# Performance work log

Measured on AMD Instinct MI355X. Metric: run time of the kernel, lower is better.

Reference implementation:

```python
import jax, jax.numpy as jnp
import numpy as np

B, S, D, H, SE, DE, DFF = 4, 1024, 1024, 16, 77, 768, 4096


def _ln(x, g, b, eps=1e-5):
    mu = jnp.mean(x, axis=-1, keepdims=True)
    var = jnp.mean((x - mu) ** 2, axis=-1, keepdims=True)
    return (x - mu) * jax.lax.rsqrt(var + eps) * g + b


def _split_heads(x, heads):
    b, s, d = x.shape
    return x.reshape(b, s, heads, d // heads).transpose(0, 2, 1, 3)  # b h s hd


def _attn(q, k, v, heads):
    # memory_efficient_attention equivalent: softmax(q k^T * scale) v, per head
    q, k, v = _split_heads(q, heads), _split_heads(k, heads), _split_heads(v, heads)
    scale = q.shape[-1] ** -0.5
    scores = jnp.einsum('bhqd,bhkd->bhqk', q, k) * scale
    probs = jax.nn.softmax(scores, axis=-1)
    o = jnp.einsum('bhqk,bhkd->bhqd', probs, v)
    b, h, s, hd = o.shape
    return o.transpose(0, 2, 1, 3).reshape(b, s, h * hd)


def _geglu_ff(x, w1, b1, w2, b2):
    proj = x @ w1 + b1
    a, gate = jnp.split(proj, 2, axis=-1)
    return (a * jax.nn.gelu(gate)) @ w2 + b2


def _forward(h1, h2, enc, wq, wk, wv, wqc, wo, bo, ln1g, ln1b, ln2g, ln2b,
             w2q, w2k, w2v, w2o, b2o, wff1, bff1, wff2, bff2):
    # norm1
    n1 = _ln(h1, ln1g[0], ln1b[0])
    n2 = _ln(h2, ln1g[1], ln1b[1])
    # dual-stream uni-direction attention (self + cross with swapped K/V)
    q1, k1, v1, q1c = n1 @ wq[0], n1 @ wk[0], n1 @ wv[0], n1 @ wqc[0]
    q2, k2, v2, q2c = n2 @ wq[1], n2 @ wk[1], n2 @ wv[1], n2 @ wqc[1]
    a1 = _attn(q1, k1, v1, H) + _attn(q1c, k2, v2, H)
    a2 = _attn(q2, k2, v2, H) + _attn(q2c, k1, v1, H)
    a1 = a1 @ wo[0] + bo[0]
    a2 = a2 @ wo[1] + bo[1]
    h1 = h1 + a1
    h2 = h2 + a2
    # cross attention to encoder states (attn2)
    n1 = _ln(h1, ln2g[0], ln2b[0])
    n2 = _ln(h2, ln2g[1], ln2b[1])
    c1 = _attn(n1 @ w2q[0], enc @ w2k[0], enc @ w2v[0], H) @ w2o[0] + b2o[0]
    c2 = _attn(n2 @ w2q[1], enc @ w2k[1], enc @ w2v[1], H) @ w2o[1] + b2o[1]
    h1 = h1 + c1
    h2 = h2 + c2
    # feed-forward (GEGLU), applied to norm2 output exactly as in source
    h1 = h1 + _geglu_ff(n1, wff1[0], bff1[0], wff2[0], bff2[0])
    h2 = h2 + _geglu_ff(n2, wff1[1], bff1[1], wff2[1], bff2[1])
    return (h1, h2)


def setup_inputs() -> dict:
    key = jax.random.key(0)
    ks = jax.random.split(key, 16)
    f = lambda k, shp: jax.random.normal(k, shp, jnp.float32) * 0.02
    return {
        'h1': jax.random.normal(ks[0], (B, S, D), jnp.float32),
        'h2': jax.random.normal(ks[1], (B, S, D), jnp.float32),
        'enc': jax.random.normal(ks[2], (B, SE, DE), jnp.float32),
        'wq': f(ks[3], (2, D, D)), 'wk': f(ks[4], (2, D, D)),
        'wv': f(ks[5], (2, D, D)), 'wqc': f(ks[6], (2, D, D)),
        'wo': f(ks[7], (2, D, D)), 'bo': jnp.zeros((2, D), jnp.float32),
        'ln1g': jnp.ones((2, D), jnp.float32), 'ln1b': jnp.zeros((2, D), jnp.float32),
        'ln2g': jnp.ones((2, D), jnp.float32), 'ln2b': jnp.zeros((2, D), jnp.float32),
        'w2q': f(ks[8], (2, D, D)), 'w2k': f(ks[9], (2, DE, D)),
        'w2v': f(ks[10], (2, DE, D)), 'w2o': f(ks[11], (2, D, D)),
        'b2o': jnp.zeros((2, D), jnp.float32),
        'wff1': f(ks[12], (2, D, 2 * DFF)), 'bff1': jnp.zeros((2, 2 * DFF), jnp.float32),
        'wff2': f(ks[13], (2, DFF, D)), 'bff2': jnp.zeros((2, D), jnp.float32),
    }


def reference(h1, h2, enc, wq, wk, wv, wqc, wo, bo, ln1g, ln1b, ln2g, ln2b,
              w2q, w2k, w2v, w2o, b2o, wff1, bff1, wff2, bff2):
    return _forward(h1, h2, enc, wq, wk, wv, wqc, wo, bo, ln1g, ln1b, ln2g, ln2b,
                    w2q, w2k, w2v, w2o, b2o, wff1, bff1, wff2, bff2)
```

## Files before the change

### kernel.cpp

```cpp
#include <hip/hip_runtime.h>

typedef unsigned short u16;
typedef short v8s __attribute__((ext_vector_type(8)));
typedef float v4f __attribute__((ext_vector_type(4)));

__device__ __forceinline__ float bf2f(u16 u) {
  union { unsigned u; float f; } c; c.u = ((unsigned)u) << 16; return c.f;
}
__device__ __forceinline__ u16 f2bf(float x) {
  union { float f; unsigned u; } c; c.f = x;
  unsigned r = c.u + 0x7fffu + ((c.u >> 16) & 1u);
  return (u16)(r >> 16);
}
__device__ __forceinline__ v4f vzero() { v4f z; z[0]=0.f; z[1]=0.f; z[2]=0.f; z[3]=0.f; return z; }
__device__ __forceinline__ v4f mfma16(v8s a, v8s b, v4f c) {
  return __builtin_amdgcn_mfma_f32_16x16x32_bf16(a, b, c, 0, 0, 0);
}
__device__ __forceinline__ void async_lds16(const void* g, void* l) {
  __builtin_amdgcn_global_load_lds((__attribute__((address_space(1))) void*)g,
                                   (__attribute__((address_space(3))) void*)l, 16, 0, 0);
}
__device__ __forceinline__ unsigned cvtpk(float lo, float hi) {
  unsigned r;
  asm("v_cvt_pk_bf16_f32 %0, %1, %2" : "=v"(r) : "v"(lo), "v"(hi));
  return r;
}
__device__ __forceinline__ float gelu_f(float x) {
  return 0.5f * x * (1.f + tanhf(0.7978845608028654f * (x + 0.044715f * x * x * x)));
}

__global__ void detect_k(const unsigned* __restrict__ p, unsigned* __restrict__ flag) {
  if (threadIdx.x == 0) {
    flag[0] = (p[0] == 0x3F803F80u) ? 1u : 0u;
    flag[1] = 0u;
  }
}

__global__ __launch_bounds__(256) void cvt_k(const unsigned* __restrict__ flag,
    const void* __restrict__ src, u16* __restrict__ dst, int n) {
  int i = (blockIdx.x * 256 + threadIdx.x) * 8;
  if (i >= n) return;
  if (*flag) {
    *(uint4*)(dst + i) = *(const uint4*)((const u16*)src + i);
  } else {
    const float* s = (const float*)src + i;
    #pragma unroll
    for (int j = 0; j < 8; ++j) dst[i + j] = f2bf(s[j]);
  }
}

__global__ __launch_bounds__(256) void tr_k(const unsigned* __restrict__ flag,
    const void* __restrict__ in, u16* __restrict__ out, int R, int C, long outZS) {
  __shared__ u16 tile[32][33];
  size_t zin = (size_t)blockIdx.z * R * C;
  size_t zout = (size_t)blockIdx.z * outZS;
  int c0 = blockIdx.x * 32, r0 = blockIdx.y * 32;
  int tx = threadIdx.x & 31, ty = threadIdx.x >> 5;
  unsigned isbf = *flag;
  const u16* inb = (const u16*)in + zin;
  const float* inf = (const float*)in + zin;
  #pragma unroll
  for (int i = ty; i < 32; i += 8) {
    size_t idx = (size_t)(r0 + i) * C + c0 + tx;
    tile[i][tx] = isbf ? inb[idx] : f2bf(inf[idx]);
  }
  __syncthreads();
  out += zout;
  #pragma unroll
  for (int i = ty; i < 32; i += 8) out[(size_t)(c0 + i) * R + r0 + tx] = tile[tx][i];
}

__global__ __launch_bounds__(256) void vtr_k(const u16* __restrict__ in, u16* __restrict__ out) {
  __shared__ u16 tile[32][33];
  int z = blockIdx.z >> 2, b = blockIdx.z & 3;
  const u16* ip = in + (size_t)z * 16777216 + (size_t)b * 4194304 + 2048;
  u16* op = out + (size_t)z * 4194304 + (size_t)b * 1048576;
  int k0 = blockIdx.x * 32, d0 = blockIdx.y * 32;
  int tx = threadIdx.x & 31, ty = threadIdx.x >> 5;
  #pragma unroll
  for (int i = ty; i < 32; i += 8)
    tile[i][tx] = ip[(size_t)(k0 + i) * 4096 + d0 + tx];
  __syncthreads();
  int sl = (((tx >> 3) & 1) << 4) | (((tx >> 2) & 1) << 3) | (((tx >> 4) & 1) << 2) | (tx & 3);
  #pragma unroll
  for (int i = ty; i < 32; i += 8)
    op[(size_t)(d0 + i) * 1024 + k0 + sl] = tile[tx][i];
}

__global__ __launch_bounds__(256) void ln_k(const unsigned* __restrict__ flag,
    const void* __restrict__ src0, const void* __restrict__ src1,
    const u16* __restrict__ gw, const u16* __restrict__ bw, u16* __restrict__ out) {
  int z = blockIdx.y;
  const void* src = z ? src1 : src0;
  out += (size_t)z * 4194304; gw += z * 1024; bw += z * 1024;
  int row = blockIdx.x, t = threadIdx.x;
  unsigned isbf = *flag;
  float4 v;
  if (isbf) {
    uint2 d = ((const uint2*)((const u16*)src + (size_t)row * 1024))[t];
    v.x = bf2f((u16)(d.x & 0xffffu)); v.y = bf2f((u16)(d.x >> 16));
    v.z = bf2f((u16)(d.y & 0xffffu)); v.w = bf2f((u16)(d.y >> 16));
  } else {
    v = ((const float4*)((const float*)src + (size_t)row * 1024))[t];
  }
  float s = v.x + v.y + v.z + v.w;
  float s2 = v.x * v.x + v.y * v.y + v.z * v.z + v.w * v.w;
  #pragma unroll
  for (int o = 32; o; o >>= 1) { s += __shfl_down(s, o); s2 += __shfl_down(s2, o); }
  __shared__ float red[8];
  int w = t >> 6;
  if ((t & 63) == 0) { red[w] = s; red[4 + w] = s2; }
  __syncthreads();
  if (t == 0) {
    red[0] = red[0] + red[1] + red[2] + red[3];
    red[4] = red[4] + red[5] + red[6] + red[7];
  }
  __syncthreads();
  float mu = red[0] * (1.f / 1024.f);
  float var = red[4] * (1.f / 1024.f) - mu * mu;
  float rstd = rsqrtf(var + 1e-5f);
  int c = t * 4;
  float xs[4] = { v.x, v.y, v.z, v.w };
  #pragma unroll
  for (int j = 0; j < 4; ++j) {
    float g = bf2f(gw[c + j]), bb = bf2f(bw[c + j]);
    out[(size_t)row * 1024 + c + j] = f2bf((xs[j] - mu) * rstd * g + bb);
  }
}

template<int EPI>
__global__ __launch_bounds__(256, 2) void gemm_bt(
    const u16* __restrict__ A, const u16* __restrict__ Bt,
    int M, int N, int K, int lda, int ldb, int ldc,
    const u16* __restrict__ bias, const u16* aux,
    float* __restrict__ resF, void* __restrict__ outB,
    long zsA, long zsB, long zsC, int zsBias,
    const void* rin0, const void* rin1,
    const unsigned* __restrict__ flagp)
{
  int z = blockIdx.z;
  A += (size_t)z * zsA;
  Bt += (size_t)z * zsB;
  size_t zc = (size_t)z * zsC;
  unsigned isbf = 0;
  if (EPI == 4 || EPI == 5) isbf = *flagp;
  const void* rin = (EPI == 5) ? (z ? rin1 : rin0) : nullptr;
  __shared__ alignas(16) u16 As[128 * 64];
  __shared__ alignas(16) u16 Bs[128 * 64];
  int tid = threadIdx.x;
  int lane = tid & 63, wave = tid >> 6;
  int l15 = lane & 15, l4 = lane >> 4;
  int wm = wave & 1, wn = wave >> 1;
  int lin = blockIdx.x + blockIdx.y * gridDim.x;
  int nxy = gridDim.x * gridDim.y;
  int sw = (lin & 7) * (nxy >> 3) + (lin >> 3);
  int bx = sw % gridDim.x, by = sw / gridDim.x;
  int m0 = bx * 128, n0 = by * 128;
  v4f acc[4][4];
  #pragma unroll
  for (int i = 0; i < 4; ++i)
    #pragma unroll
    for (int j = 0; j < 4; ++j) acc[i][j] = vzero();

  for (int k0 = 0; k0 < K; k0 += 64) {
    #pragma unroll
    for (int it = 0; it < 4; ++it) {
      int sidx = it * 256 + tid;
      int r = sidx >> 3, cs = (sidx & 7) * 8;
      int ra = m0 + r; if (ra > M - 1) ra = M - 1;
      async_lds16(A + (size_t)ra * lda + k0 + cs, As + (size_t)(it * 256 + wave * 64) * 8);
      async_lds16(Bt + (size_t)(n0 + r) * ldb + k0 + cs, Bs + (size_t)(it * 256 + wave * 64) * 8);
    }
    __syncthreads();
    #pragma unroll
    for (int ks = 0; ks < 2; ++ks) {
      v8s af[4], bfr[4];
      #pragma unroll
      for (int i = 0; i < 4; ++i) {
        af[i]  = *(const v8s*)(As + (wm * 64 + i * 16 + l15) * 64 + ks * 32 + l4 * 8);
        bfr[i] = *(const v8s*)(Bs + (wn * 64 + i * 16 + l15) * 64 + ks * 32 + l4 * 8);
      }
      #pragma unroll
      for (int i = 0; i < 4; ++i)
        #pragma unroll
        for (int j = 0; j < 4; ++j)
          acc[i][j] = mfma16(af[i], bfr[j], acc[i][j]);
    }
    __syncthreads();
  }
  #pragma unroll
  for (int mt = 0; mt < 4; ++mt) {
    #pragma unroll
    for (int r = 0; r < 4; ++r) {
      int gr = m0 + wm * 64 + mt * 16 + l4 * 4 + r;
      if (gr >= M) continue;
      size_t ri = (size_t)gr * ldc;
      size_t ro = zc + ri;
      #pragma unroll
      for (int nt = 0; nt < 4; ++nt) {
        int gc = n0 + wn * 64 + nt * 16 + l15;
        float v = acc[mt][nt][r];
        if (bias) v += bf2f(bias[(size_t)z * zsBias + gc]);
        if (EPI == 0) ((u16*)outB)[ro + gc] = f2bf(v);
        else if (EPI == 1) ((u16*)outB)[ro + gc] = f2bf(gelu_f(v));
        else if (EPI == 2) ((u16*)outB)[ro + gc] = f2bf(v * bf2f(aux[ro + gc]));
        else if (EPI == 3) resF[ro + gc] += v;
        else if (EPI == 5) {
          float h = isbf ? bf2f(((const u16*)rin)[ri + gc]) : ((const float*)rin)[ri + gc];
          resF[ro + gc] = h + v;
        } else {
          float o = resF[ro + gc] + v;
          if (isbf) ((u16*)outB)[ro + gc] = f2bf(o);
          else ((float*)outB)[ro + gc] = o;
        }
      }
    }
  }
}

template<int EPI>
__global__ __launch_bounds__(512, 2) void gemm256(
    const u16* __restrict__ A, const u16* __restrict__ Bt,
    int M, int N, int K, int lda, int ldb, int ldc,
    const u16* __restrict__ bias, const u16* aux, void* __restrict__ outB,
    long zsA, long zsB, long zsC, int zsBias)
{
  __shared__ alignas(16) u16 As[4][8192];
  __shared__ alignas(16) u16 Bs[4][8192];
  int z = blockIdx.z;
  A += (size_t)z * zsA;
  Bt += (size_t)z * zsB;
  size_t zc = (size_t)z * zsC;
  int tid = threadIdx.x, lane = tid & 63, wave = tid >> 6;
  int l15 = lane & 15, l4 = lane >> 4;
  int wm = wave >> 2, wn = wave & 3;
  int lin = blockIdx.x + blockIdx.y * gridDim.x;
  int nxy = gridDim.x * gridDim.y;
  int sw = (lin & 7) * (nxy >> 3) + (lin >> 3);
  int bx = sw % gridDim.x, by = sw / gridDim.x;
  int m0 = bx * 256, n0 = by * 256;
  int sa = l4 ^ ((l15 >> 1) & 3);
  int nG = K >> 5;

  v4f acc[8][4];
  #pragma unroll
  for (int i = 0; i < 8; ++i)
    #pragma unroll
    for (int j = 0; j < 4; ++j) acc[i][j] = vzero();

  auto stage = [&](int g) {
    int sl = g & 3;
    #pragma unroll
    for (int l = 0; l < 2; ++l) {
      int sidx = l * 512 + tid;
      int r = sidx >> 2, c = sidx & 3;
      int cs = (c ^ ((sidx >> 3) & 3)) * 8;
      async_lds16(A + (size_t)(m0 + r) * lda + g * 32 + cs,
                  As[sl] + (size_t)(l * 512 + wave * 64) * 8);
      async_lds16(Bt + (size_t)(n0 + r) * ldb + g * 32 + cs,
                  Bs[sl] + (size_t)(l * 512 + wave * 64) * 8);
    }
  };
  auto gate = [&](int cnt) {
    if (cnt >= 2)      asm volatile("s_waitcnt vmcnt(8)" ::: "memory");
    else if (cnt == 1) asm volatile("s_waitcnt vmcnt(4)" ::: "memory");
    else               asm volatile("s_waitcnt vmcnt(0)" ::: "memory");
    __builtin_amdgcn_sched_barrier(0);
  };
  v8s FA[8], FB[8], Bf[4];
  auto dsA = [&](v8s* F, int u) {
    const u16* a = As[u & 3];
    #pragma unroll
    for (int i = 0; i < 8; ++i)
      F[i] = *(const v8s*)(a + ((wm * 128 + i * 16 + l15) * 4 + sa) * 8);
  };
  auto dsB = [&](int u) {
    const u16* bp = Bs[u & 3];
    #pragma unroll
    for (int j = 0; j < 4; ++j)
      Bf[j] = *(const v8s*)(bp + ((wn * 64 + j * 16 + l15) * 4 + sa) * 8);
  };
  auto lgk = [&](bool more) {
    if (more) asm volatile("s_waitcnt lgkmcnt(8)" ::: "memory");
    else      asm volatile("s_waitcnt lgkmcnt(0)" ::: "memory");
    __builtin_amdgcn_sched_barrier(0);
  };
  auto mfma_blk = [&](v8s* F) {
    __builtin_amdgcn_s_setprio(1);
    #pragma unroll
    for (int i = 0; i < 8; ++i)
      #pragma unroll
      for (int j = 0; j < 4; ++j) acc[i][j] = mfma16(F[i], Bf[j], acc[i][j]);
    __builtin_amdgcn_s_setprio(0);
  };

  stage(0);
  if (1 < nG) stage(1);
  if (2 < nG) stage(2);
  gate((1 < nG) + (2 < nG));
  __builtin_amdgcn_s_barrier();
  dsA(FA, 0);

  for (int u = 0; u < nG; u += 2) {
    if (u + 3 < nG) stage(u + 3);
    gate((u + 2 < nG) + (u + 3 < nG));
    __builtin_amdgcn_s_barrier();
    dsB(u);
    if (u + 1 < nG) dsA(FB, u + 1);
    lgk(u + 1 < nG);
    mfma_blk(FA);
    __builtin_amdgcn_s_barrier();
    if (u + 1 < nG) {
      if (u + 4 < nG) stage(u + 4);
      gate((u + 3 < nG) + (u + 4 < nG));
      __builtin_amdgcn_s_barrier();
      dsB(u + 1);
      if (u + 2 < nG) dsA(FA, u + 2);
      lgk(u + 2 < nG);
      mfma_blk(FB);
      __builtin_amdgcn_s_barrier();
    }
  }

  #pragma unroll
  for (int mi = 0; mi < 8; ++mi) {
    #pragma unroll
    for (int rr = 0; rr < 4; ++rr) {
      int gr = m0 + wm * 128 + mi * 16 + l4 * 4 + rr;
      size_t ro = zc + (size_t)gr * ldc;
      #pragma unroll
      for (int ni = 0; ni < 4; ++ni) {
        int gc = n0 + wn * 64 + ni * 16 + l15;
        float v = acc[mi][ni][rr];
        if (bias) v += bf2f(bias[(size_t)z * zsBias + gc]);
        if (EPI == 0) ((u16*)outB)[ro + gc] = f2bf(v);
        else if (EPI == 1) ((u16*)outB)[ro + gc] = f2bf(gelu_f(v));
        else ((u16*)outB)[ro + gc] = f2bf(v * bf2f(aux[ro + gc]));
      }
    }
  }
}

__global__ __launch_bounds__(256, 4) void flash_self_k(
    const u16* __restrict__ qkv, const u16* __restrict__ Vt, u16* __restrict__ O)
{
  __shared__ alignas(16) u16 Ksh[128 * 64];
  __shared__ alignas(16) u16 Vsh[64 * 128];
  int tid = threadIdx.x, lane = tid & 63, wave = tid >> 6;
  int l15 = lane & 15, l4 = (lane >> 4) & 3;
  int lin = blockIdx.x + (blockIdx.y << 4) + (blockIdx.z << 8);
  int sw = (lin & 7) * 256 + (lin >> 3);
  int qblk = sw & 15, h = (sw >> 4) & 15, zb = sw >> 8;
  int strm = zb >> 2, b = zb & 3;
  const size_t ZS = 16777216;
  const size_t BS = 4194304;
  int q0 = qblk * 64 + wave * 16;
  int swz = l15 & 7;
  v4f res[4];
  #pragma unroll
  for (int i = 0; i < 4; ++i) res[i] = vzero();

  for (int sg = 0; sg < 2; ++sg) {
    int qcol = sg ? 3072 : 0;
    int ksrc = sg ? (strm ^ 1) : strm;
    const u16* Qb = qkv + (size_t)strm * ZS + (size_t)b * BS + qcol + h * 64;
    const u16* Kb = qkv + (size_t)ksrc * ZS + (size_t)b * BS + 1024 + h * 64;
    const u16* Vb = Vt + (size_t)ksrc * BS + (size_t)b * 1048576 + h * 65536;
    v8s qf0 = *(const v8s*)(Qb + (size_t)(q0 + l15) * 4096 + l4 * 8);
    v8s qf1 = *(const v8s*)(Qb + (size_t)(q0 + l15) * 4096 + l4 * 8 + 32);
    v4f oacc[4];
    #pragma unroll
    for (int i = 0; i < 4; ++i) oacc[i] = vzero();
    float mrun = -1e30f, lrun = 0.f;

    for (int c0 = 0; c0 < 1024; c0 += 128) {
      #pragma unroll
      for (int it = 0; it < 4; ++it) {
        int sidx = it * 256 + tid;
        int r = sidx >> 3, c = sidx & 7;
        async_lds16(Kb + (size_t)(c0 + r) * 4096 + ((c ^ (r & 7)) * 8),
                    Ksh + (size_t)(it * 256 + wave * 64) * 8);
      }
      #pragma unroll
      for (int it = 0; it < 4; ++it) {
        int sidx = it * 256 + tid;
        int d = sidx >> 4, c = sidx & 15;
        async_lds16(Vb + (size_t)d * 1024 + c0 + ((c ^ (d & 15)) * 8),
                    Vsh + (size_t)(it * 256 + wave * 64) * 8);
      }
      __syncthreads();
      v4f s[4][2];
      #pragma unroll
      for (int g = 0; g < 4; ++g) { s[g][0] = vzero(); s[g][1] = vzero(); }
      __builtin_amdgcn_s_setprio(1);
      #pragma unroll
      for (int g = 0; g < 4; ++g) {
        int rb0 = (g * 32 + l15) * 64, rb1 = rb0 + 16 * 64;
        v8s k00 = *(const v8s*)(Ksh + rb0 + ((l4 ^ swz) * 8));
        v8s k10 = *(const v8s*)(Ksh + rb1 + ((l4 ^ swz) * 8));
        v8s k01 = *(const v8s*)(Ksh + rb0 + (((4 + l4) ^ swz) * 8));
        v8s k11 = *(const v8s*)(Ksh + rb1 + (((4 + l4) ^ swz) * 8));
        s[g][0] = mfma16(k00, qf0, s[g][0]);
        s[g][1] = mfma16(k10, qf0, s[g][1]);
        s[g][0] = mfma16(k01, qf1, s[g][0]);
        s[g][1] = mfma16(k11, qf1, s[g][1]);
      }
      __builtin_amdgcn_s_setprio(0);
      float tm = -1e30f;
      #pragma unroll
      for (int g = 0; g < 4; ++g)
        #pragma unroll
        for (int hh = 0; hh < 2; ++hh)
          #pragma unroll
          for (int r = 0; r < 4; ++r) {
            s[g][hh][r] *= 0.125f;
            tm = fmaxf(tm, s[g][hh][r]);
          }
      tm = fmaxf(tm, __shfl_xor(tm, 16));
      tm = fmaxf(tm, __shfl_xor(tm, 32));
      float alpha = 1.f;
      if (!__all(tm <= mrun + 8.f)) {
        float mn = fmaxf(mrun, tm);
        alpha = __expf(mrun - mn);
        mrun = mn;
        #pragma unroll
        for (int r = 0; r < 4; ++r) {
          float ar = __shfl(alpha, l4 * 4 + r);
          #pragma unroll
          for (int nt = 0; nt < 4; ++nt) oacc[nt][r] *= ar;
        }
      }
      float rs = 0.f;
      unsigned pk[4][4];
      #pragma unroll
      for (int g = 0; g < 4; ++g)
        #pragma unroll
        for (int hh = 0; hh < 2; ++hh) {
          float p0 = __expf(s[g][hh][0] - mrun);
          float p1 = __expf(s[g][hh][1] - mrun);
          float p2 = __expf(s[g][hh][2] - mrun);
          float p3 = __expf(s[g][hh][3] - mrun);
          rs += (p0 + p1) + (p2 + p3);
          pk[g][hh * 2]     = cvtpk(p0, p1);
          pk[g][hh * 2 + 1] = cvtpk(p2, p3);
        }
      rs += __shfl_xor(rs, 16);
      rs += __shfl_xor(rs, 32);
      lrun = lrun * alpha + rs;
      __builtin_amdgcn_s_setprio(1);
      #pragma unroll
      for (int g = 0; g < 4; ++g) {
        union { unsigned u[4]; v8s v; } pa;
        pa.u[0] = pk[g][0]; pa.u[1] = pk[g][1]; pa.u[2] = pk[g][2]; pa.u[3] = pk[g][3];
        #pragma unroll
        for (int nt = 0; nt < 4; ++nt) {
          int vr = nt * 16 + l15;
          v8s vb = *(const v8s*)(Vsh + vr * 128 + (((g * 4 + l4) ^ (vr & 15)) * 8));
          oacc[nt] = mfma16(pa.v, vb, oacc[nt]);
        }
      }
      __builtin_amdgcn_s_setprio(0);
      __syncthreads();
    }
    #pragma unroll
    for (int r = 0; r < 4; ++r) {
      float lr = __shfl(lrun, l4 * 4 + r);
      float inv = 1.f / lr;
      #pragma unroll
      for (int nt = 0; nt < 4; ++nt) res[nt][r] += oacc[nt][r] * inv;
    }
  }
  #pragma unroll
  for (int nt = 0; nt < 4; ++nt) {
    #pragma unroll
    for (int r = 0; r < 4; ++r) {
      int gq = q0 + l4 * 4 + r;
      size_t oi = (size_t)strm * BS + ((size_t)b * 1024 + gq) * 1024 + h * 64 + nt * 16 + l15;
      O[oi] = f2bf(res[nt][r]);
    }
  }
}

__global__ __launch_bounds__(256, 2) void flash_cross_k(
    const u16* __restrict__ Q, const u16* __restrict__ KV, u16* __restrict__ O)
{
  __shared__ alignas(16) u16 Ksh[128 * 64];
  __shared__ alignas(16) unsigned VshT[64 * 68];
  __shared__ alignas(16) u16 Psh[4][16 * 128];
  int tid = threadIdx.x, lane = tid & 63, wave = tid >> 6;
  int l15 = lane & 15, l4 = lane >> 4;
  int h = blockIdx.y;
  int strm = blockIdx.z >> 2, b = blockIdx.z & 3;
  const u16* Qb = Q + (size_t)strm * 4194304 + (size_t)b * 1048576 + h * 64;
  const u16* Kb = KV + (size_t)strm * 630784 + (size_t)b * 157696 + h * 64;
  const u16* Vb = Kb + 1024;
  int q0 = blockIdx.x * 64 + wave * 16;
  u16* pw = Psh[wave];
  int swz = l15 & 7;
  v8s qf0 = *(const v8s*)(Qb + (size_t)(q0 + l15) * 1024 + l4 * 8);
  v8s qf1 = *(const v8s*)(Qb + (size_t)(q0 + l15) * 1024 + l4 * 8 + 32);

  #pragma unroll
  for (int it = 0; it < 4; ++it) {
    int sidx = it * 256 + tid;
    int r = sidx >> 3, c = sidx & 7;
    int gk = r > 76 ? 76 : r;
    async_lds16(Kb + (size_t)gk * 2048 + ((c ^ (r & 7)) * 8),
                Ksh + (size_t)(it * 256 + wave * 64) * 8);
  }
  #pragma unroll
  for (int it = 0; it < 2; ++it) {
    int tt = it * 256 + tid;
    int kp = tt & 63, dsg = tt >> 6;
    int gk0 = kp * 2, gk1 = kp * 2 + 1;
    if (gk0 > 76) gk0 = 76;
    if (gk1 > 76) gk1 = 76;
    v8s v0 = *(const v8s*)(Vb + (size_t)gk0 * 2048 + dsg * 8);
    v8s v1 = *(const v8s*)(Vb + (size_t)gk1 * 2048 + dsg * 8);
    #pragma unroll
    for (int j = 0; j < 8; ++j) {
      unsigned pk = (unsigned)(u16)v0[j] | ((unsigned)(u16)v1[j] << 16);
      VshT[(dsg * 8 + j) * 68 + kp] = pk;
    }
  }
  __syncthreads();
  v4f s[4][2];
  #pragma unroll
  for (int g = 0; g < 4; ++g) { s[g][0] = vzero(); s[g][1] = vzero(); }
  __builtin_amdgcn_s_setprio(1);
  #pragma unroll
  for (int g = 0; g < 4; ++g) {
    int rb0 = (g * 32 + l15) * 64, rb1 = rb0 + 16 * 64;
    v8s k00 = *(const v8s*)(Ksh + rb0 + ((l4 ^ swz) * 8));
    v8s k10 = *(const v8s*)(Ksh + rb1 + ((l4 ^ swz) * 8));
    v8s k01 = *(const v8s*)(Ksh + rb0 + (((4 + l4) ^ swz) * 8));
    v8s k11 = *(const v8s*)(Ksh + rb1 + (((4 + l4) ^ swz) * 8));
    s[g][0] = mfma16(qf0, k00, s[g][0]);
    s[g][1] = mfma16(qf0, k10, s[g][1]);
    s[g][0] = mfma16(qf1, k01, s[g][0]);
    s[g][1] = mfma16(qf1, k11, s[g][1]);
  }
  __builtin_amdgcn_s_setprio(0);
  float lsum[4];
  #pragma unroll
  for (int r = 0; r < 4; ++r) {
    int row = l4 * 4 + r;
    float x[8];
    #pragma unroll
    for (int g = 0; g < 4; ++g) {
      bool ok0 = (g * 32 + l15) < 77, ok1 = (g * 32 + 16 + l15) < 77;
      x[2 * g]     = ok0 ? s[g][0][r] * 0.125f : -1e30f;
      x[2 * g + 1] = ok1 ? s[g][1][r] * 0.125f : -1e30f;
    }
    float tm = fmaxf(fmaxf(fmaxf(x[0], x[1]), fmaxf(x[2], x[3])),
                     fmaxf(fmaxf(x[4], x[5]), fmaxf(x[6], x[7])));
    #pragma unroll
    for (int o = 8; o; o >>= 1) tm = fmaxf(tm, __shfl_xor(tm, o));
    float rs = 0.f;
    #pragma unroll
    for (int j = 0; j < 8; ++j) {
      float p = __expf(x[j] - tm);
      rs += p;
      int col = (j >> 1) * 32 + (j & 1) * 16 + l15;
      pw[row * 128 + (((col >> 3) ^ row) * 8) + (col & 7)] = f2bf(p);
    }
    #pragma unroll
    for (int o = 8; o; o >>= 1) rs += __shfl_xor(rs, o);
    lsum[r] = rs;
  }
  v4f oacc[4];
  #pragma unroll
  for (int i = 0; i < 4; ++i) oacc[i] = vzero();
  __builtin_amdgcn_s_setprio(1);
  #pragma unroll
  for (int g = 0; g < 4; ++g) {
    v8s pa = *(const v8s*)(pw + l15 * 128 + (((g * 4 + l4) ^ l15) * 8));
    #pragma unroll
    for (int nt = 0; nt < 4; ++nt) {
      v8s vb = *(const v8s*)((const u16*)VshT + (nt * 16 + l15) * 136 + g * 32 + l4 * 8);
      oacc[nt] = mfma16(pa, vb, oacc[nt]);
    }
  }
  __builtin_amdgcn_s_setprio(0);
  #pragma unroll
  for (int nt = 0; nt < 4; ++nt) {
    #pragma unroll
    for (int r = 0; r < 4; ++r) {
      int gq = q0 + l4 * 4 + r;
      size_t oi = (size_t)strm * 4194304 + ((size_t)b * 1024 + gq) * 1024 + h * 64 + nt * 16 + l15;
      O[oi] = f2bf(oacc[nt][r] / lsum[r]);
    }
  }
}

extern "C" void kernel_launch(void* const* d_in, const int* in_sizes, int n_in,
                              void* d_out, int out_size, void* d_ws, size_t ws_size,
                              hipStream_t stream)
{
  (void)in_sizes; (void)n_in; (void)out_size;
  const void* h1   = d_in[0];
  const void* h2   = d_in[1];
  const void* enc  = d_in[2];
  const void* wq   = d_in[3];
  const void* wk   = d_in[4];
  const void* wv   = d_in[5];
  const void* wqc  = d_in[6];
  const void* wo   = d_in[7];
  const void* bo   = d_in[8];
  const void* ln1g = d_in[9];
  const void* ln1b = d_in[10];
  const void* ln2g = d_in[11];
  const void* ln2b = d_in[12];
  const void* w2q  = d_in[13];
  const void* w2k  = d_in[14];
  const void* w2v  = d_in[15];
  const void* w2o  = d_in[16];
  const void* b2o  = d_in[17];
  const void* wff1 = d_in[18];
  const void* bff1 = d_in[19];
  const void* wff2 = d_in[20];
  const void* bff2 = d_in[21];

  const size_t S1 = 4194304;
  const size_t W1 = 1048576;
  const size_t QS = 16777216;
  const size_t NE = 236544;

  char* base = (char*)d_ws;
  size_t off = 0;
  auto AL = [&](size_t n) { size_t r = off; off += (n + 255) & ~(size_t)255; return r; };
  size_t o_flag   = AL(256);
  size_t o_pb     = AL(30720 * 2);
  size_t o_encB   = AL(NE * 2);
  size_t o_wqkvT  = AL(2 * 4 * W1 * 2);
  size_t o_woT    = AL(2 * W1 * 2);
  size_t o_w2qT   = AL(2 * W1 * 2);
  size_t o_w2oT   = AL(2 * W1 * 2);
  size_t o_w2kvT  = AL(2 * 2048 * 768 * 2);
  size_t o_wff1T  = AL(2 * 8192 * 1024 * 2);
  size_t o_wff2T  = AL(2 * 4096 * 1024 * 2);
  size_t o_hw     = AL(2 * S1 * 4);
  size_t o_n      = AL(2 * S1 * 2);
  size_t o_qkv    = AL(2 * QS * 2);
  size_t o_ab     = AL(2 * S1 * 2);
  if (ws_size < off) return;

  unsigned* flagp = (unsigned*)(base + o_flag);
  const unsigned* zerop = flagp + 1;
  u16* pb = (u16*)(base + o_pb);
  u16* boB   = pb + 0;
  u16* b2oB  = pb + 2048;
  u16* ln1gB = pb + 4096;
  u16* ln1bB = pb + 6144;
  u16* ln2gB = pb + 8192;
  u16* ln2bB = pb + 10240;
  u16* bff2B = pb + 12288;
  u16* bff1B = pb + 14336;
  u16* encB  = (u16*)(base + o_encB);
  u16* wqkvT = (u16*)(base + o_wqkvT);
  u16* woT   = (u16*)(base + o_woT);
  u16* w2qT  = (u16*)(base + o_w2qT);
  u16* w2oT  = (u16*)(base + o_w2oT);
  u16* w2kvT = (u16*)(base + o_w2kvT);
  u16* wff1T = (u16*)(base + o_wff1T);
  u16* wff2T = (u16*)(base + o_wff2T);
  float* hw  = (float*)(base + o_hw);
  u16* n1    = (u16*)(base + o_n);
  u16* qkv   = (u16*)(base + o_qkv);
  u16* a1b   = (u16*)(base + o_ab);
  u16* q1x   = qkv;
  u16* c1b   = qkv + 2 * S1;
  u16* kencv = qkv + 4 * S1;
  u16* gelu  = qkv;
  u16* vtb   = n1;

  auto tr = [&](const void* ip, u16* op, int R, int C, long outZS) {
    dim3 g(C / 32, R / 32, 2);
    tr_k<<<g, 256, 0, stream>>>(flagp, ip, op, R, C, outZS);
  };
  auto cvt = [&](const void* ip, u16* op, int n) {
    cvt_k<<<(n / 8 + 255) / 256, 256, 0, stream>>>(flagp, ip, op, n);
  };
  auto gemm = [&](int epi, const u16* Ap, const u16* Bp, int M, int N, int K,
                  int lda, int ldb, int ldc, const u16* bias, const u16* aux,
                  float* resF, void* oB, int nz, long zsA, long zsB, long zsC, int zsBias,
                  const void* rin0, const void* rin1) {
    dim3 g((M + 127) / 128, N / 128, nz);
    switch (epi) {
      case 0: gemm_bt<0><<<g, 256, 0, stream>>>(Ap, Bp, M, N, K, lda, ldb, ldc, bias, aux, resF, oB, zsA, zsB, zsC, zsBias, rin0, rin1, flagp); break;
      case 1: gemm_bt<1><<<g, 256, 0, stream>>>(Ap, Bp, M, N, K, lda, ldb, ldc, bias, aux, resF, oB, zsA, zsB, zsC, zsBias, rin0, rin1, flagp); break;
      case 2: gemm_bt<2><<<g, 256, 0, stream>>>(Ap, Bp, M, N, K, lda, ldb, ldc, bias, aux, resF, oB, zsA, zsB, zsC, zsBias, rin0, rin1, flagp); break;
      case 3: gemm_bt<3><<<g, 256, 0, stream>>>(Ap, Bp, M, N, K, lda, ldb, ldc, bias, aux, resF, oB, zsA, zsB, zsC, zsBias, rin0, rin1, flagp); break;
      case 4: gemm_bt<4><<<g, 256, 0, stream>>>(Ap, Bp, M, N, K, lda, ldb, ldc, bias, aux, resF, oB, zsA, zsB, zsC, zsBias, rin0, rin1, flagp); break;
      default: gemm_bt<5><<<g, 256, 0, stream>>>(Ap, Bp, M, N, K, lda, ldb, ldc, bias, aux, resF, oB, zsA, zsB, zsC, zsBias, rin0, rin1, flagp); break;
    }
  };

  detect_k<<<1, 64, 0, stream>>>((const unsigned*)ln1g, flagp);
  cvt(bo, boB, 2048);     cvt(b2o, b2oB, 2048);
  cvt(ln1g, ln1gB, 2048); cvt(ln1b, ln1bB, 2048);
  cvt(ln2g, ln2gB, 2048); cvt(ln2b, ln2bB, 2048);
  cvt(bff2, bff2B, 2048); cvt(bff1, bff1B, 16384);
  cvt(enc, encB, (int)NE);
  tr(wq,  wqkvT + 0 * W1, 1024, 1024, 4 * (long)W1);
  tr(wk,  wqkvT + 1 * W1, 1024, 1024, 4 * (long)W1);
  tr(wv,  wqkvT + 2 * W1, 1024, 1024, 4 * (long)W1);
  tr(wqc, wqkvT + 3 * W1, 1024, 1024, 4 * (long)W1);
  tr(wo,  woT,  1024, 1024, (long)W1);
  tr(w2q, w2qT, 1024, 1024, (long)W1);
  tr(w2o, w2oT, 1024, 1024, (long)W1);
  tr(w2k, w2kvT + 0,          768, 1024, 2048L * 768);
  tr(w2v, w2kvT + 1024 * 768, 768, 1024, 2048L * 768);
  tr(wff1, wff1T, 1024, 8192, 8192L * 1024);
  tr(wff2, wff2T, 4096, 1024, 4096L * 1024);
  ln_k<<<dim3(4096, 2), 256, 0, stream>>>(flagp, h1, h2, ln1gB, ln1bB, n1);
  gemm256<0><<<dim3(16, 16, 2), 512, 0, stream>>>(n1, wqkvT, 4096, 4096, 1024,
      1024, 1024, 4096, nullptr, nullptr, qkv, (long)S1, 4 * (long)W1, (long)QS, 0);
  vtr_k<<<dim3(32, 32, 8), 256, 0, stream>>>(qkv, vtb);
  flash_self_k<<<dim3(16, 16, 8), 256, 0, stream>>>(qkv, vtb, a1b);
  gemm(5, a1b, woT, 4096, 1024, 1024, 1024, 1024, 1024, boB, nullptr, hw, nullptr,
       2, (long)S1, (long)W1, (long)S1, 1024, h1, h2);
  ln_k<<<dim3(4096, 2), 256, 0, stream>>>(zerop, hw, hw + S1, ln2gB, ln2bB, n1);
  gemm(0, n1, w2qT, 4096, 1024, 1024, 1024, 1024, 1024, nullptr, nullptr, nullptr, q1x,
       2, (long)S1, (long)W1, (long)S1, 0, nullptr, nullptr);
  gemm(0, encB, w2kvT, 308, 2048, 768, 768, 768, 2048, nullptr, nullptr, nullptr, kencv,
       2, 0, 2048L * 768, 308L * 2048, 0, nullptr, nullptr);
  flash_cross_k<<<dim3(16, 16, 8), 256, 0, stream>>>(q1x, kencv, c1b);
  gemm(3, c1b, w2oT, 4096, 1024, 1024, 1024, 1024, 1024, b2oB, nullptr, hw, nullptr,
       2, (long)S1, (long)W1, (long)S1, 1024, nullptr, nullptr);
  gemm256<1><<<dim3(16, 16, 2), 512, 0, stream>>>(n1, wff1T + 4096 * 1024, 4096, 4096, 1024,
      1024, 1024, 4096, bff1B + 4096, nullptr, gelu, (long)S1, 8192L * 1024, (long)QS, 8192);
  gemm256<2><<<dim3(16, 16, 2), 512, 0, stream>>>(n1, wff1T, 4096, 4096, 1024,
      1024, 1024, 4096, bff1B, gelu, gelu, (long)S1, 8192L * 1024, (long)QS, 8192);
  gemm(4, gelu, wff2T, 4096, 1024, 4096, 4096, 4096, 1024,
       bff2B, nullptr, hw, d_out, 2, (long)QS, 4096L * 1024, (long)S1, 1024,
       nullptr, nullptr);
}
```

Measured before the change: 1.198 ms.

## Restructure gemm256 main loop into K-64 double-buffered eight-phase schedule

Replaces the four-slot K-32 ring buffer in the 256x256 GEMM with a double-buffered K-64 tile. Each tile is split into two K-32 halves, and each half into two M halves, giving four compute phases per tile. Global-to-LDS async loads for later tiles are interleaved between the phases, and each wave keeps only four A fragments live instead of two sets of eight, which lowers register pressure. The cost is more barriers and full lgkmcnt waits per tile. The loop also assumes K is a multiple of 64.

```diff
diff --git a/kernel.cpp b/kernel.cpp
--- a/kernel.cpp
+++ b/kernel.cpp
@@ -225,8 +225,8 @@
     const u16* __restrict__ bias, const u16* aux, void* __restrict__ outB,
     long zsA, long zsB, long zsC, int zsBias)
 {
-  __shared__ alignas(16) u16 As[4][8192];
-  __shared__ alignas(16) u16 Bs[4][8192];
+  __shared__ alignas(16) u16 Asl[2][2][256 * 32];
+  __shared__ alignas(16) u16 Bsl[2][2][256 * 32];
   int z = blockIdx.z;
   A += (size_t)z * zsA;
   Bt += (size_t)z * zsB;
@@ -240,7 +240,7 @@
   int bx = sw % gridDim.x, by = sw / gridDim.x;
   int m0 = bx * 256, n0 = by * 256;
   int sa = l4 ^ ((l15 >> 1) & 3);
-  int nG = K >> 5;
+  int Kt = K >> 6;
 
   v4f acc[8][4];
   #pragma unroll
@@ -248,78 +248,90 @@
     #pragma unroll
     for (int j = 0; j < 4; ++j) acc[i][j] = vzero();
 
-  auto stage = [&](int g) {
-    int sl = g & 3;
+  auto stA = [&](int g, int ks) {
+    u16* dst = Asl[g & 1][ks];
     #pragma unroll
     for (int l = 0; l < 2; ++l) {
       int sidx = l * 512 + tid;
       int r = sidx >> 2, c = sidx & 3;
-      int cs = (c ^ ((sidx >> 3) & 3)) * 8;
-      async_lds16(A + (size_t)(m0 + r) * lda + g * 32 + cs,
-                  As[sl] + (size_t)(l * 512 + wave * 64) * 8);
-      async_lds16(Bt + (size_t)(n0 + r) * ldb + g * 32 + cs,
-                  Bs[sl] + (size_t)(l * 512 + wave * 64) * 8);
-    }
-  };
-  auto gate = [&](int cnt) {
-    if (cnt >= 2)      asm volatile("s_waitcnt vmcnt(8)" ::: "memory");
-    else if (cnt == 1) asm volatile("s_waitcnt vmcnt(4)" ::: "memory");
-    else               asm volatile("s_waitcnt vmcnt(0)" ::: "memory");
+      async_lds16(A + (size_t)(m0 + r) * lda + g * 64 + ks * 32 + ((c ^ ((r >> 1) & 3)) * 8),
+                  dst + (size_t)(l * 512 + wave * 64) * 8);
+    }
+  };
+  auto stB = [&](int g, int ks) {
+    u16* dst = Bsl[g & 1][ks];
+    #pragma unroll
+    for (int l = 0; l < 2; ++l) {
+      int sidx = l * 512 + tid;
+      int r = sidx >> 2, c = sidx & 3;
+      async_lds16(Bt + (size_t)(n0 + r) * ldb + g * 64 + ks * 32 + ((c ^ ((r >> 1) & 3)) * 8),
+                  dst + (size_t)(l * 512 + wave * 64) * 8);
+    }
+  };
+  auto gate = [&](bool deep) {
+    if (deep) asm volatile("s_waitcnt vmcnt(6)" ::: "memory");
+    else      asm volatile("s_waitcnt vmcnt(0)" ::: "memory");
     __builtin_amdgcn_sched_barrier(0);
   };
-  v8s FA[8], FB[8], Bf[4];
-  auto dsA = [&](v8s* F, int u) {
-    const u16* a = As[u & 3];
-    #pragma unroll
-    for (int i = 0; i < 8; ++i)
-      F[i] = *(const v8s*)(a + ((wm * 128 + i * 16 + l15) * 4 + sa) * 8);
-  };
-  auto dsB = [&](int u) {
-    const u16* bp = Bs[u & 3];
+  auto lgk0 = [&]() {
+    asm volatile("s_waitcnt lgkmcnt(0)" ::: "memory");
+    __builtin_amdgcn_sched_barrier(0);
+  };
+  v8s Af[4], Bf[4];
+  auto ldA = [&](int db, int ks, int mh) {
+    const u16* a = Asl[db][ks];
+    #pragma unroll
+    for (int i = 0; i < 4; ++i)
+      Af[i] = *(const v8s*)(a + ((wm * 128 + mh * 64 + i * 16 + l15) * 4 + sa) * 8);
+  };
+  auto ldB = [&](int db, int ks) {
+    const u16* b = Bsl[db][ks];
     #pragma unroll
     for (int j = 0; j < 4; ++j)
-      Bf[j] = *(const v8s*)(bp + ((wn * 64 + j * 16 + l15) * 4 + sa) * 8);
-  };
-  auto lgk = [&](bool more) {
-    if (more) asm volatile("s_waitcnt lgkmcnt(8)" ::: "memory");
-    else      asm volatile("s_waitcnt lgkmcnt(0)" ::: "memory");
-    __builtin_amdgcn_sched_barrier(0);
-  };
-  auto mfma_blk = [&](v8s* F) {
+      Bf[j] = *(const v8s*)(b + ((wn * 64 + j * 16 + l15) * 4 + sa) * 8);
+  };
+  auto mf = [&](int mh) {
     __builtin_amdgcn_s_setprio(1);
     #pragma unroll
-    for (int i = 0; i < 8; ++i)
-      #pragma unroll
-      for (int j = 0; j < 4; ++j) acc[i][j] = mfma16(F[i], Bf[j], acc[i][j]);
+    for (int i = 0; i < 4; ++i)
+      #pragma unroll
+      for (int j = 0; j < 4; ++j)
+        acc[mh * 4 + i][j] = mfma16(Af[i], Bf[j], acc[mh * 4 + i][j]);
     __builtin_amdgcn_s_setprio(0);
   };
 
-  stage(0);
-  if (1 < nG) stage(1);
-  if (2 < nG) stage(2);
-  gate((1 < nG) + (2 < nG));
+  stB(0, 0); stA(0, 0); stB(0, 1); stA(0, 1);
+  if (Kt > 1) { stB(1, 0); stA(1, 0); stB(1, 1); }
+  gate(Kt > 1);
   __builtin_amdgcn_s_barrier();
-  dsA(FA, 0);
-
-  for (int u = 0; u < nG; u += 2) {
-    if (u + 3 < nG) stage(u + 3);
-    gate((u + 2 < nG) + (u + 3 < nG));
+
+  for (int t = 0; t < Kt; ++t) {
+    int db = t & 1;
+    ldA(db, 0, 0); ldB(db, 0);
+    if (t + 1 < Kt) stA(t + 1, 1);
     __builtin_amdgcn_s_barrier();
-    dsB(u);
-    if (u + 1 < nG) dsA(FB, u + 1);
-    lgk(u + 1 < nG);
-    mfma_blk(FA);
+    lgk0();
+    mf(0);
     __builtin_amdgcn_s_barrier();
-    if (u + 1 < nG) {
-      if (u + 4 < nG) stage(u + 4);
-      gate((u + 3 < nG) + (u + 4 < nG));
-      __builtin_amdgcn_s_barrier();
-      dsB(u + 1);
-      if (u + 2 < nG) dsA(FA, u + 2);
-      lgk(u + 2 < nG);
-      mfma_blk(FB);
-      __builtin_amdgcn_s_barrier();
-    }
+    ldA(db, 0, 1);
+    if (t + 2 < Kt) stB(t + 2, 0);
+    __builtin_amdgcn_s_barrier();
+    lgk0();
+    mf(1);
+    __builtin_amdgcn_s_barrier();
+    ldA(db, 1, 0); ldB(db, 1);
+    if (t + 2 < Kt) stA(t + 2, 0);
+    __builtin_amdgcn_s_barrier();
+    lgk0();
+    mf(0);
+    __builtin_amdgcn_s_barrier();
+    ldA(db, 1, 1);
+    if (t + 2 < Kt) stB(t + 2, 1);
+    __builtin_amdgcn_s_barrier();
+    lgk0();
+    mf(1);
+    gate(t + 2 < Kt);
+    __builtin_amdgcn_s_barrier();
   }
 
   #pragma unroll
```

Result: faster. 1.123 ms (-6.3%).
